# Kernel tuning notes

Measured on AMD Instinct MI355X. Metric: run time of the kernel, lower is better.

The kernel has to match this reference:

```python
import jax, jax.numpy as jnp
import numpy as np

N_NODES = 50000
N_EDGES = 800000
D_IN = 64
D_OUT = 64
N_REL = 8


def setup_inputs() -> dict:
    key = jax.random.key(0)
    ks = jax.random.split(key, 7)
    x = jax.random.normal(ks[0], (N_NODES, D_IN), jnp.float32)
    src = jax.random.randint(ks[1], (N_EDGES,), 0, N_NODES)   # neighbor ids
    dst = jax.random.randint(ks[2], (N_EDGES,), 0, N_NODES)   # center node ids
    rel = jax.random.randint(ks[3], (N_EDGES,), 0, N_REL)
    # xavier_uniform for W_r: [R, 2*d, d]
    lim = float(np.sqrt(6.0 / (2 * D_IN + D_IN)))
    W_r = jax.random.uniform(ks[4], (N_REL, 2 * D_IN, D_IN), jnp.float32, -lim, lim)
    # nn.Linear(2*d, d_out): weight [d_out, 2*d], bias [d_out]
    lim2 = float(1.0 / np.sqrt(2 * D_IN))
    W_lin = jax.random.uniform(ks[5], (D_OUT, 2 * D_IN), jnp.float32, -lim2, lim2)
    b_lin = jax.random.uniform(ks[6], (D_OUT,), jnp.float32, -lim2, lim2)
    return {"x": x, "src": src, "dst": dst, "rel": rel,
            "W_r": W_r, "W_lin": W_lin, "b_lin": b_lin}


def reference(x, src, dst, rel, W_r, W_lin, b_lin):
    n, d = x.shape
    e = src.shape[0]
    # gate logit per edge: (concat(x[dst], x[src]) @ W_r[rel]).sum(-1)
    # == concat(x[dst], x[src]) . W_r[rel].sum(-1)  -- mathematically identical,
    # avoids materializing the [E, 2d, d] matmul the torch loop performs.
    w = W_r.sum(-1)                      # [R, 2d]
    w_dst, w_src = w[:, :d], w[:, d:]    # [R, d] each
    logit = jnp.sum(x[dst] * w_dst[rel], axis=-1) + jnp.sum(x[src] * w_src[rel], axis=-1)  # [E]
    gate = jax.nn.sigmoid(logit)[:, None]        # [E, 1]
    weighted = x[src] * gate                     # [E, d]
    # scatter-mean over destination nodes (nodes with no edges stay zero)
    agg_sum = jax.ops.segment_sum(weighted, dst, num_segments=n)            # [N, d]
    cnt = jax.ops.segment_sum(jnp.ones((e,), x.dtype), dst, num_segments=n)  # [N]
    agg = agg_sum / jnp.maximum(cnt, 1.0)[:, None]
    combined = jnp.concatenate([x, agg], axis=-1)  # [N, 2d]
    out = combined @ W_lin.T + b_lin               # [N, d_out]
    return jax.nn.leaky_relu(out, negative_slope=0.01)
```

## Files before the change

kernel.cpp:

```cpp
#include <hip/hip_runtime.h>
#include <cmath>

#define N_NODES 50000
#define N_EDGES 800000
#define D 64
#define N_REL 8

#define NODES_PER_BLK 32
#define TN 16
#define CPAD 16
#define MAXDEG 64

static __device__ __forceinline__ unsigned f2bf(float f) {
    unsigned u = __float_as_uint(f);
    return (u + 0x7FFFu + ((u >> 16) & 1u)) >> 16;
}
#define BFLO(u) __uint_as_float((u) << 16)
#define BFHI(u) __uint_as_float((u) & 0xFFFF0000u)

__global__ void wprep_kernel(const float* __restrict__ W_r, float* __restrict__ w,
                             int* __restrict__ cnt) {
    int t = blockIdx.x * blockDim.x + threadIdx.x;
    if (t < N_REL * 2 * D) {
        const float* p = W_r + (size_t)t * D;
        float s = 0.0f;
#pragma unroll
        for (int k = 0; k < D; ++k) s += p[k];
        w[t] = s;
    }
    for (int i = t; i < N_NODES * CPAD; i += gridDim.x * blockDim.x)
        cnt[i] = 0;
}

__global__ __launch_bounds__(256) void tables_kernel(
    const float* __restrict__ x, const float* __restrict__ w,
    float* __restrict__ Dn, float* __restrict__ Sr,
    unsigned short* __restrict__ xb)
{
    __shared__ float xs[TN][68];
    __shared__ float ws[16][68];

    int tid = threadIdx.x;
    int n0  = blockIdx.x * TN;

    for (int i = tid; i < 16 * 64; i += 256)
        ws[i >> 6][i & 63] = w[i];
    for (int i = tid; i < TN * 64; i += 256) {
        int n = n0 + (i >> 6);
        xs[i >> 6][i & 63] = (n < N_NODES) ? x[(size_t)n * D + (i & 63)] : 0.f;
    }
    __syncthreads();

    for (int i = tid; i < TN * 64; i += 256) {
        int n = n0 + (i >> 6);
        if (n < N_NODES) xb[(size_t)n0 * D + i] = (unsigned short)f2bf(xs[i >> 6][i & 63]);
    }

    int q = tid & 15, nl = tid >> 4;
    float acc = 0.f;
#pragma unroll
    for (int k = 0; k < 64; k += 4) {
        float4 a = *(const float4*)&xs[nl][k];
        float4 b = *(const float4*)&ws[q][k];
        acc += a.x * b.x + a.y * b.y + a.z * b.z + a.w * b.w;
    }
    int n = n0 + nl;
    if (n < N_NODES) {
        int r = q >> 1;
        if ((q & 1) == 0) Dn[n * 8 + r] = acc;
        else              Sr[n * 8 + r] = acc;
    }
}

__global__ void scatter_kernel(const int* __restrict__ src, const int* __restrict__ dst,
                               const int* __restrict__ rel,
                               int* __restrict__ cnt,
                               const float* __restrict__ Dn, const float* __restrict__ Sr,
                               float2* __restrict__ epack) {
    int e = blockIdx.x * blockDim.x + threadIdx.x;
    if (e >= N_EDGES) return;
    int s = src[e], d = dst[e], r = rel[e];
    float logit = Dn[d * 8 + r] + Sr[s * 8 + r];
    float gate = 1.0f / (1.0f + __expf(-logit));
    int rank = atomicAdd(&cnt[d * CPAD], 1);
    if (rank < MAXDEG) {
        float2 v; v.x = gate; v.y = __int_as_float(s);
        epack[(size_t)d * MAXDEG + rank] = v;
    }
}

__global__ __launch_bounds__(256) void agg_kernel(
    const unsigned short* __restrict__ xb,
    const int*   __restrict__ cnt,
    const float2* __restrict__ epack,
    unsigned int* __restrict__ aggb)
{
    int n    = (blockIdx.x * blockDim.x + threadIdx.x) >> 6;
    int lane = threadIdx.x & 63;
    if (n >= N_NODES) return;

    int sub = lane >> 4;
    int q   = lane & 15;
    int deg = cnt[n * CPAD];
    int m   = (deg < MAXDEG) ? deg : MAXDEG;
    int beg = n * MAXDEG;
    int end = beg + m;

    float ax = 0.f, ay = 0.f, az = 0.f, aw = 0.f;

    for (int base = beg; base < end; base += 8) {
        int e0 = base + sub;
        int e1 = base + 4 + sub;
        float g0 = 0.f, g1 = 0.f;
        int   s0 = 0,   s1 = 0;
        if (e0 < end) { float2 v = epack[e0]; g0 = v.x; s0 = __float_as_int(v.y); }
        if (e1 < end) { float2 v = epack[e1]; g1 = v.x; s1 = __float_as_int(v.y); }
        uint2 u0 = {0u, 0u}, u1 = {0u, 0u};
        if (e0 < end) u0 = *(const uint2*)&xb[(size_t)s0 * D + 4 * q];
        if (e1 < end) u1 = *(const uint2*)&xb[(size_t)s1 * D + 4 * q];
        ax += g0 * BFLO(u0.x) + g1 * BFLO(u1.x);
        ay += g0 * BFHI(u0.x) + g1 * BFHI(u1.x);
        az += g0 * BFLO(u0.y) + g1 * BFLO(u1.y);
        aw += g0 * BFHI(u0.y) + g1 * BFHI(u1.y);
    }

#pragma unroll
    for (int off = 16; off <= 32; off <<= 1) {
        ax += __shfl_xor(ax, off, 64);
        ay += __shfl_xor(ay, off, 64);
        az += __shfl_xor(az, off, 64);
        aw += __shfl_xor(aw, off, 64);
    }

    if (sub == 0) {
        float inv = 1.0f / fmaxf((float)deg, 1.0f);
        uint2 pr;
        pr.x = f2bf(ax * inv) | (f2bf(ay * inv) << 16);
        pr.y = f2bf(az * inv) | (f2bf(aw * inv) << 16);
        *(uint2*)&aggb[(size_t)n * 32 + 2 * q] = pr;
    }
}

__global__ __launch_bounds__(256, 6) void lin_kernel(
    const unsigned int* __restrict__ xbu,
    const unsigned int* __restrict__ aggb,
    const float* __restrict__ W_lin,
    const float* __restrict__ b_lin,
    float* __restrict__ out)
{
    __shared__ unsigned int W2[64][66];
    __shared__ unsigned int c2[NODES_PER_BLK][66];
    __shared__ float b_lds[64];

    int tid = threadIdx.x;
    int n0  = blockIdx.x * NODES_PER_BLK;

    for (int i = tid; i < 64 * 64; i += 256) {
        int j = i >> 6, kp = i & 63;
        float2 wv = *(const float2*)&W_lin[j * 128 + kp * 2];
        W2[j][kp] = f2bf(wv.x) | (f2bf(wv.y) << 16);
    }
    if (tid < 64) b_lds[tid] = b_lin[tid];

    for (int i = tid; i < NODES_PER_BLK * 32; i += 256) {
        int nl = i >> 5, kp = i & 31;
        int n  = n0 + nl;
        unsigned vx = 0u, va = 0u;
        if (n < N_NODES) {
            vx = xbu[(size_t)n * 32 + kp];
            va = aggb[(size_t)n * 32 + kp];
        }
        c2[nl][kp]      = vx;
        c2[nl][32 + kp] = va;
    }
    __syncthreads();

    int tx = tid & 15, ty = tid >> 4;
    float acc[2][4];
#pragma unroll
    for (int i = 0; i < 2; ++i)
#pragma unroll
        for (int jj = 0; jj < 4; ++jj) acc[i][jj] = b_lds[tx + 16 * jj];

#pragma unroll 2
    for (int kp = 0; kp < 64; kp += 2) {
        uint2 cu[2], wu[4];
        cu[0] = *(const uint2*)&c2[ty][kp];
        cu[1] = *(const uint2*)&c2[ty + 16][kp];
#pragma unroll
        for (int jj = 0; jj < 4; ++jj)
            wu[jj] = *(const uint2*)&W2[tx + 16 * jj][kp];
#pragma unroll
        for (int i = 0; i < 2; ++i) {
            float cx = BFLO(cu[i].x), cy = BFHI(cu[i].x);
            float cz = BFLO(cu[i].y), cw = BFHI(cu[i].y);
#pragma unroll
            for (int jj = 0; jj < 4; ++jj) {
                acc[i][jj] += cx * BFLO(wu[jj].x) + cy * BFHI(wu[jj].x)
                            + cz * BFLO(wu[jj].y) + cw * BFHI(wu[jj].y);
            }
        }
    }

#pragma unroll
    for (int i = 0; i < 2; ++i) {
        int n = n0 + ty + 16 * i;
        if (n < N_NODES) {
#pragma unroll
            for (int jj = 0; jj < 4; ++jj) {
                float v = acc[i][jj];
                out[(size_t)n * D + tx + 16 * jj] = (v > 0.f) ? v : 0.01f * v;
            }
        }
    }
}

extern "C" void kernel_launch(void* const* d_in, const int* in_sizes, int n_in,
                              void* d_out, int out_size, void* d_ws, size_t ws_size,
                              hipStream_t stream) {
    const float* x     = (const float*)d_in[0];
    const int*   src   = (const int*)  d_in[1];
    const int*   dst   = (const int*)  d_in[2];
    const int*   rel   = (const int*)  d_in[3];
    const float* W_r   = (const float*)d_in[4];
    const float* W_lin = (const float*)d_in[5];
    const float* b_lin = (const float*)d_in[6];
    float* out = (float*)d_out;

    char* p = (char*)d_ws;
    float*  w       = (float*)p;                p += 4096;
    float*  Dn      = (float*)p;                p += (size_t)N_NODES * 8 * 4;
    float*  Sr      = (float*)p;                p += (size_t)N_NODES * 8 * 4;
    int*    cnt     = (int*)p;                  p += (size_t)N_NODES * CPAD * 4;
    float2* epack   = (float2*)p;               p += (size_t)N_NODES * MAXDEG * 8;
    unsigned short* xb = (unsigned short*)p;    p += (size_t)N_NODES * D * 2;
    unsigned int* aggb = (unsigned int*)p;      p += (size_t)N_NODES * 32 * 4;

    wprep_kernel<<<512, 256, 0, stream>>>(W_r, w, cnt);
    tables_kernel<<<(N_NODES + TN - 1) / TN, 256, 0, stream>>>(x, w, Dn, Sr, xb);
    scatter_kernel<<<(N_EDGES + 255) / 256, 256, 0, stream>>>(src, dst, rel, cnt,
                                                              Dn, Sr, epack);
    agg_kernel<<<(N_NODES * 64 + 255) / 256, 256, 0, stream>>>(xb, cnt, epack, aggb);
    lin_kernel<<<(N_NODES + NODES_PER_BLK - 1) / NODES_PER_BLK, 256, 0, stream>>>(
        (const unsigned int*)xb, aggb, W_lin, b_lin, out);
}
```

Before: 191.8 us.

## Bin edges by destination segment before building per-node edge lists

Replaces the single scatter kernel with two passes. The first computes gates and bins packed edge records into 8 buckets by destination-node range, using a shared-memory local sort. The second replays each bucket to do the per-node count atomics and epack writes, so those atomics and scattered writes stay within a cache-sized node range. This costs an extra global write and read of the packed records, packs src and dst into 16 bits each, and drops edges if a bucket exceeds its fixed capacity.

```diff
diff --git a/kernel.cpp b/kernel.cpp
--- a/kernel.cpp
+++ b/kernel.cpp
@@ -10,6 +10,12 @@
 #define TN 16
 #define CPAD 16
 #define MAXDEG 64
+#define NSEG 8
+#define SEG_DIV 6250
+#define EPB 1024
+#define NBLK_BIN ((N_EDGES + EPB - 1) / EPB)
+#define BUCKET_CAP 102400
+#define SLICES 64
 
 static __device__ __forceinline__ unsigned f2bf(float f) {
     unsigned u = __float_as_uint(f);
@@ -19,7 +25,7 @@
 #define BFHI(u) __uint_as_float((u) & 0xFFFF0000u)
 
 __global__ void wprep_kernel(const float* __restrict__ W_r, float* __restrict__ w,
-                             int* __restrict__ cnt) {
+                             int* __restrict__ cnt, int* __restrict__ bucket_cnt) {
     int t = blockIdx.x * blockDim.x + threadIdx.x;
     if (t < N_REL * 2 * D) {
         const float* p = W_r + (size_t)t * D;
@@ -28,6 +34,7 @@
         for (int k = 0; k < D; ++k) s += p[k];
         w[t] = s;
     }
+    if (t < NSEG) bucket_cnt[t] = 0;
     for (int i = t; i < N_NODES * CPAD; i += gridDim.x * blockDim.x)
         cnt[i] = 0;
 }
@@ -72,20 +79,90 @@
     }
 }
 
-__global__ void scatter_kernel(const int* __restrict__ src, const int* __restrict__ dst,
-                               const int* __restrict__ rel,
-                               int* __restrict__ cnt,
-                               const float* __restrict__ Dn, const float* __restrict__ Sr,
-                               float2* __restrict__ epack) {
-    int e = blockIdx.x * blockDim.x + threadIdx.x;
-    if (e >= N_EDGES) return;
-    int s = src[e], d = dst[e], r = rel[e];
-    float logit = Dn[d * 8 + r] + Sr[s * 8 + r];
-    float gate = 1.0f / (1.0f + __expf(-logit));
-    int rank = atomicAdd(&cnt[d * CPAD], 1);
-    if (rank < MAXDEG) {
-        float2 v; v.x = gate; v.y = __int_as_float(s);
-        epack[(size_t)d * MAXDEG + rank] = v;
+__global__ __launch_bounds__(256) void bin_kernel(
+    const int* __restrict__ src, const int* __restrict__ dst,
+    const int* __restrict__ rel,
+    const float* __restrict__ Dn, const float* __restrict__ Sr,
+    int* __restrict__ bucket_cnt,
+    unsigned long long* __restrict__ buckets)
+{
+    __shared__ unsigned long long buf[EPB];
+    __shared__ int hist[NSEG], runoff[NSEG + 1], place[NSEG], gbase[NSEG];
+
+    int tid = threadIdx.x;
+    int e0  = blockIdx.x * EPB;
+
+    if (tid < NSEG) hist[tid] = 0;
+    __syncthreads();
+
+    unsigned long long rec[4];
+    int seg[4];
+    int cntl = 0;
+#pragma unroll
+    for (int j = 0; j < 4; ++j) {
+        int e = e0 + tid + j * 256;
+        if (e < N_EDGES) {
+            int s = src[e], d = dst[e], r = rel[e];
+            float logit = Dn[d * 8 + r] + Sr[s * 8 + r];
+            float gate = 1.0f / (1.0f + __expf(-logit));
+            rec[cntl] = ((unsigned long long)__float_as_uint(gate) << 32)
+                      | ((unsigned)d << 16) | (unsigned)s;
+            seg[cntl] = d / SEG_DIV;
+            atomicAdd(&hist[seg[cntl]], 1);
+            ++cntl;
+        }
+    }
+    __syncthreads();
+
+    if (tid == 0) {
+        int acc = 0;
+        for (int k = 0; k < NSEG; ++k) { runoff[k] = acc; place[k] = acc; acc += hist[k]; }
+        runoff[NSEG] = acc;
+    }
+    __syncthreads();
+
+    for (int j = 0; j < cntl; ++j) {
+        int p = atomicAdd(&place[seg[j]], 1);
+        buf[p] = rec[j];
+    }
+    if (tid < NSEG) gbase[tid] = atomicAdd(&bucket_cnt[tid], hist[tid]);
+    __syncthreads();
+
+    int total = runoff[NSEG];
+    for (int i = tid; i < total; i += 256) {
+        int k = 0;
+        while (k < NSEG - 1 && i >= runoff[k + 1]) ++k;
+        int pos = gbase[k] + (i - runoff[k]);
+        if (pos < BUCKET_CAP)
+            buckets[(size_t)k * BUCKET_CAP + pos] = buf[i];
+    }
+}
+
+__global__ __launch_bounds__(256) void build_kernel(
+    const int* __restrict__ bucket_cnt,
+    const unsigned long long* __restrict__ buckets,
+    int* __restrict__ cnt,
+    float2* __restrict__ epack)
+{
+    int s     = blockIdx.x & (NSEG - 1);
+    int slice = blockIdx.x >> 3;
+    int m = bucket_cnt[s];
+    if (m > BUCKET_CAP) m = BUCKET_CAP;
+    int per = (m + SLICES - 1) / SLICES;
+    int b0 = slice * per;
+    int b1 = b0 + per; if (b1 > m) b1 = m;
+    const unsigned long long* B = buckets + (size_t)s * BUCKET_CAP;
+
+    for (int i = b0 + threadIdx.x; i < b1; i += 256) {
+        unsigned long long pk = B[i];
+        int sI = (int)(pk & 0xFFFFu);
+        int d  = (int)((pk >> 16) & 0xFFFFu);
+        float gate = __uint_as_float((unsigned)(pk >> 32));
+        int rank = atomicAdd(&cnt[d * CPAD], 1);
+        if (rank < MAXDEG) {
+            float2 v; v.x = gate; v.y = __int_as_float(sI);
+            epack[(size_t)d * MAXDEG + rank] = v;
+        }
     }
 }
 
@@ -228,18 +305,21 @@
     float* out = (float*)d_out;
 
     char* p = (char*)d_ws;
-    float*  w       = (float*)p;                p += 4096;
-    float*  Dn      = (float*)p;                p += (size_t)N_NODES * 8 * 4;
-    float*  Sr      = (float*)p;                p += (size_t)N_NODES * 8 * 4;
-    int*    cnt     = (int*)p;                  p += (size_t)N_NODES * CPAD * 4;
-    float2* epack   = (float2*)p;               p += (size_t)N_NODES * MAXDEG * 8;
+    float*  w        = (float*)p;               p += 4096;
+    float*  Dn       = (float*)p;               p += (size_t)N_NODES * 8 * 4;
+    float*  Sr       = (float*)p;               p += (size_t)N_NODES * 8 * 4;
+    int*    cnt      = (int*)p;                 p += (size_t)N_NODES * CPAD * 4;
+    int*    bucket_cnt = (int*)p;               p += 256;
+    unsigned long long* buckets = (unsigned long long*)p;
+                                                p += (size_t)NSEG * BUCKET_CAP * 8;
+    float2* epack    = (float2*)p;              p += (size_t)N_NODES * MAXDEG * 8;
     unsigned short* xb = (unsigned short*)p;    p += (size_t)N_NODES * D * 2;
     unsigned int* aggb = (unsigned int*)p;      p += (size_t)N_NODES * 32 * 4;
 
-    wprep_kernel<<<512, 256, 0, stream>>>(W_r, w, cnt);
+    wprep_kernel<<<512, 256, 0, stream>>>(W_r, w, cnt, bucket_cnt);
     tables_kernel<<<(N_NODES + TN - 1) / TN, 256, 0, stream>>>(x, w, Dn, Sr, xb);
-    scatter_kernel<<<(N_EDGES + 255) / 256, 256, 0, stream>>>(src, dst, rel, cnt,
-                                                              Dn, Sr, epack);
+    bin_kernel<<<NBLK_BIN, 256, 0, stream>>>(src, dst, rel, Dn, Sr, bucket_cnt, buckets);
+    build_kernel<<<NSEG * SLICES, 256, 0, stream>>>(bucket_cnt, buckets, cnt, epack);
     agg_kernel<<<(N_NODES * 64 + 255) / 256, 256, 0, stream>>>(xb, cnt, epack, aggb);
     lin_kernel<<<(N_NODES + NODES_PER_BLK - 1) / NODES_PER_BLK, 256, 0, stream>>>(
         (const unsigned int*)xb, aggb, W_lin, b_lin, out);
```

Result: slower. 199.1 us (+3.8%).
